# Performance work log

Measured on AMD Instinct MI355X. Metric: run time of the kernel, lower is better.

The kernel has to match this reference:

```python
import jax, jax.numpy as jnp
import numpy as np

B, L, HID, H, DH, M = 4, 4096, 1024, 16, 64, 128
EPS = 1e-3  # numerical_stabilizer


def setup_inputs() -> dict:
    key = jax.random.key(0)
    ks = jax.random.split(key, 7)
    lim = float(np.sqrt(6.0 / (HID + HID)))
    return {
        "query_input": jax.random.normal(ks[0], (B, L, HID), jnp.float32),
        "source_input": jax.random.normal(ks[1], (B, L, HID), jnp.float32),
        "Wq": jax.random.uniform(ks[2], (HID, H, DH), jnp.float32, -lim, lim),
        "Wk": jax.random.uniform(ks[3], (HID, H, DH), jnp.float32, -lim, lim),
        "Wv": jax.random.uniform(ks[4], (HID, H, DH), jnp.float32, -lim, lim),
        "Wo": jax.random.uniform(ks[5], (H, DH, HID), jnp.float32, -lim, lim),
        "proj": jax.random.normal(ks[6], (M, DH), jnp.float32),
        "training": 0,
    }


def _relu_kernel(x, proj):
    # relu_kernel_transformation: ratio * relu(x @ proj^T) + eps, [B,L,H,M]
    ratio = 1.0 / float(np.sqrt(proj.shape[0]))
    return jax.nn.relu(ratio * jnp.einsum("blhd,md->blhm", x, proj)) + EPS


def reference(query_input, source_input, Wq, Wk, Wv, Wo, proj, training):
    # QKV projections (DenseEinsum, no bias): [B,L,HID] -> [B,L,H,DH]
    q = jnp.einsum("bld,dhk->blhk", query_input, Wq)
    k = jnp.einsum("bld,dhk->blhk", source_input, Wk)
    v = jnp.einsum("bld,dhk->blhk", source_input, Wv)

    qp = _relu_kernel(q, proj)  # [B,L,H,M]
    kp = _relu_kernel(k, proj)  # [B,L,H,M]

    # noncausal FAVOR+: numerator via kv aggregation, linear in L
    kvs = jnp.einsum("blhm,blhd->bhmd", kp, v)          # [B,H,M,DH]
    num = jnp.einsum("blhm,bhmd->blhd", qp, kvs)        # [B,L,H,DH]
    ks_sum = jnp.sum(kp, axis=1)                         # [B,H,M]
    den = jnp.einsum("blhm,bhm->blh", qp, ks_sum)       # [B,L,H]
    att = num / den[..., None]                           # [B,L,H,DH]

    # output projection: [B,L,H,DH] -> [B,L,HID]
    return jnp.einsum("blhd,hdk->blk", att, Wo)
```

## Files before the change

### kernel.cpp

```cpp
#include <hip/hip_runtime.h>
#include <hip/hip_bf16.h>

#define B_   4
#define L_   4096
#define HID_ 1024
#define H_   16
#define DH_  64
#define M_   128
#define BL_  (B_*L_)
#define NROW (BL_*H_)

using short8 = __attribute__((ext_vector_type(8))) short;
using f32x4  = __attribute__((ext_vector_type(4))) float;

__device__ __forceinline__ float b2f(ushort s) {
    return __builtin_bit_cast(float, (unsigned int)s << 16);
}
__device__ __forceinline__ ushort f2b(float f) {
    unsigned int u = __builtin_bit_cast(unsigned int, f);
    u += 0x7fffu + ((u >> 16) & 1u);
    return (ushort)(u >> 16);
}

__device__ __forceinline__ void gld16(void* lds, const void* g) {
    __builtin_amdgcn_global_load_lds(
        (const __attribute__((address_space(1))) unsigned int*)g,
        (__attribute__((address_space(3))) unsigned int*)lds, 16, 0, 0);
}

__device__ __forceinline__ void xcd_swz_4x64(int& bx, int& by) {
    int orig = (int)blockIdx.x + ((int)blockIdx.y << 2);
    int nu = ((orig & 7) << 5) + (orig >> 3);
    bx = nu & 3; by = nu >> 2;
}

__device__ __forceinline__ void xcd_swz_8x128(int& bx, int& by) {
    int orig = (int)blockIdx.x + ((int)blockIdx.y << 3);
    int nu = ((orig & 7) << 7) + (orig >> 3);
    bx = nu & 7; by = nu >> 3;
}

__device__ __forceinline__ void gemm256_core(
    const ushort* __restrict__ A, const ushort* __restrict__ BT,
    int sA, int sB, ushort* LA, ushort* LB, f32x4 acc[8][4])
{
    const int t = threadIdx.x, w = t >> 6, lane = t & 63;
    const int wm = w >> 2, wn = w & 3, kg = lane >> 4, lr = lane & 15;
    const ushort* ga = A  + (size_t)lane * sA + w * 8;
    const ushort* gb = BT + (size_t)lane * sB + w * 8;
    ushort* la = LA + (size_t)(w * 256) * 8;
    ushort* lb = LB + (size_t)(w * 256) * 8;

    auto stageA = [&](int buf, int kt) {
        const ushort* g = ga + kt * 64;
        ushort* l = la + buf * 16384;
        #pragma unroll
        for (int j = 0; j < 4; ++j)
            gld16(l + (size_t)j * 512, g + (size_t)j * 64 * sA);
    };
    auto stageB = [&](int buf, int kt) {
        const ushort* g = gb + kt * 64;
        ushort* l = lb + buf * 16384;
        #pragma unroll
        for (int j = 0; j < 4; ++j)
            gld16(l + (size_t)j * 512, g + (size_t)j * 64 * sB);
    };
    auto compute = [&](int buf, int q) {
        const int kk = q >> 1, mh = q & 1;
        const ushort* lA_ = LA + buf * 16384;
        const ushort* lB_ = LB + buf * 16384;
        short8 av[4], bv[4];
        #pragma unroll
        for (int i = 0; i < 4; ++i)
            av[i] = *(const short8*)(lA_ +
                ((size_t)(kk*4 + kg)*256 + wm*128 + mh*64 + i*16 + lr) * 8);
        #pragma unroll
        for (int i = 0; i < 4; ++i)
            bv[i] = *(const short8*)(lB_ +
                ((size_t)(kk*4 + kg)*256 + wn*64 + i*16 + lr) * 8);
        __builtin_amdgcn_s_setprio(1);
        #pragma unroll
        for (int i = 0; i < 4; ++i)
            #pragma unroll
            for (int j = 0; j < 4; ++j)
                acc[mh*4 + i][j] = __builtin_amdgcn_mfma_f32_16x16x32_bf16(
                    av[i], bv[j], acc[mh*4 + i][j], 0, 0, 0);
        __builtin_amdgcn_s_setprio(0);
    };

    stageA(0, 0); stageB(0, 0);
    for (int kt = 0; kt < 16; ++kt) {
        const int buf = kt & 1;
        __syncthreads();
        compute(buf, 0);
        if (kt < 15) stageA(buf ^ 1, kt + 1);
        compute(buf, 1);
        if (kt < 15) stageB(buf ^ 1, kt + 1);
        compute(buf, 2);
        compute(buf, 3);
    }
    __syncthreads();
}

__device__ __forceinline__ void zero84(f32x4 acc[8][4]) {
    const f32x4 z4 = {0.f, 0.f, 0.f, 0.f};
    #pragma unroll
    for (int i = 0; i < 8; ++i)
        #pragma unroll
        for (int j = 0; j < 4; ++j) acc[i][j] = z4;
}

__global__ __launch_bounds__(512) void gemm_phi_mfma256(
    const ushort* __restrict__ A, const ushort* __restrict__ BT,
    const float* __restrict__ proj, ushort* __restrict__ OUT)
{
    __shared__ __align__(16) ushort lds[65536];
    int bx, by; xcd_swz_4x64(bx, by);
    const int bm = by * 256, bn = bx * 256, h0 = bx * 4;

    f32x4 acc[8][4];
    zero84(acc);
    gemm256_core(A + (size_t)bm * HID_, BT + (size_t)bn * HID_,
                 HID_, HID_, lds, lds + 32768, acc);

    const int t = threadIdx.x, w = t >> 6, lane = t & 63;
    const int wm = w >> 2, wn = w & 3, lr = lane & 15, rq = lane >> 4;

    short8 pbv[2][2];
    #pragma unroll
    for (int kk = 0; kk < 2; ++kk)
        #pragma unroll
        for (int n2 = 0; n2 < 2; ++n2) {
            const float* p = proj + (size_t)(wn*32 + n2*16 + lr) * DH_
                                  + (kk*4 + rq) * 8;
            float4 x = *(const float4*)p, y = *(const float4*)(p + 4);
            short8 v;
            v[0]=(short)f2b(x.x); v[1]=(short)f2b(x.y);
            v[2]=(short)f2b(x.z); v[3]=(short)f2b(x.w);
            v[4]=(short)f2b(y.x); v[5]=(short)f2b(y.y);
            v[6]=(short)f2b(y.z); v[7]=(short)f2b(y.w);
            pbv[kk][n2] = v;
        }

    #pragma unroll
    for (int mt = 0; mt < 8; ++mt)
        #pragma unroll
        for (int nt = 0; nt < 4; ++nt)
            #pragma unroll
            for (int p = 0; p < 4; ++p) {
                int row = wm*128 + mt*16 + rq*4 + p;
                int d   = nt*16 + lr;
                lds[(size_t)wn*16384 + ((size_t)(d>>3)*256 + row)*8 + (d&7)]
                    = f2b(acc[mt][nt][p]);
            }
    __syncthreads();

    const float ratio = 0.08838834764831845f;
    #pragma unroll
    for (int hs = 0; hs < 4; ++hs) {
        f32x4 a2[8][2];
        const f32x4 z4 = {0.f, 0.f, 0.f, 0.f};
        #pragma unroll
        for (int i = 0; i < 8; ++i) { a2[i][0] = z4; a2[i][1] = z4; }
        #pragma unroll
        for (int kk = 0; kk < 2; ++kk)
            #pragma unroll
            for (int mt = 0; mt < 8; ++mt) {
                short8 av = *(const short8*)(lds + (size_t)hs*16384 +
                    ((size_t)(kk*4 + rq)*256 + wm*128 + mt*16 + lr) * 8);
                #pragma unroll
                for (int n2 = 0; n2 < 2; ++n2)
                    a2[mt][n2] = __builtin_amdgcn_mfma_f32_16x16x32_bf16(
                        av, pbv[kk][n2], a2[mt][n2], 0, 0, 0);
            }
        #pragma unroll
        for (int mt = 0; mt < 8; ++mt)
            #pragma unroll
            for (int n2 = 0; n2 < 2; ++n2)
                #pragma unroll
                for (int p = 0; p < 4; ++p) {
                    size_t rowg = bm + wm*128 + mt*16 + rq*4 + p;
                    int m = wn*32 + n2*16 + lr;
                    float v = fmaxf(a2[mt][n2][p] * ratio, 0.f) + 1e-3f;
                    OUT[(rowg * H_ + (h0 + hs)) * M_ + m] = f2b(v);
                }
    }
}

__global__ __launch_bounds__(512) void gemm256_bf16(
    const ushort* __restrict__ A, const ushort* __restrict__ BT,
    ushort* __restrict__ C)
{
    __shared__ __align__(16) ushort lds[65536];
    int bx, by; xcd_swz_4x64(bx, by);
    const int bm = by * 256, bn = bx * 256;
    f32x4 acc[8][4];
    zero84(acc);
    gemm256_core(A + (size_t)bm * HID_, BT + (size_t)bn * HID_,
                 HID_, HID_, lds, lds + 32768, acc);
    const int t = threadIdx.x, w = t >> 6, lane = t & 63;
    const int wm = w >> 2, wn = w & 3, lr = lane & 15, rq = lane >> 4;
    #pragma unroll
    for (int mt = 0; mt < 8; ++mt)
        #pragma unroll
        for (int nt = 0; nt < 4; ++nt)
            #pragma unroll
            for (int p = 0; p < 4; ++p) {
                size_t row = bm + wm*128 + mt*16 + rq*4 + p;
                int col = bn + wn*64 + nt*16 + lr;
                C[row * HID_ + col] = f2b(acc[mt][nt][p]);
            }
}

__global__ __launch_bounds__(512) void gemm256_f32(
    const ushort* __restrict__ A, const ushort* __restrict__ BT,
    float* __restrict__ C)
{
    __shared__ __align__(16) ushort lds[65536];
    int bx, by; xcd_swz_4x64(bx, by);
    const int bm = by * 256, bn = bx * 256;
    f32x4 acc[8][4];
    zero84(acc);
    gemm256_core(A + (size_t)bm * HID_, BT + (size_t)bn * HID_,
                 HID_, HID_, lds, lds + 32768, acc);
    const int t = threadIdx.x, w = t >> 6, lane = t & 63;
    const int wm = w >> 2, wn = w & 3, lr = lane & 15, rq = lane >> 4;
    #pragma unroll
    for (int mt = 0; mt < 8; ++mt)
        #pragma unroll
        for (int nt = 0; nt < 4; ++nt)
            #pragma unroll
            for (int p = 0; p < 4; ++p) {
                size_t row = bm + wm*128 + mt*16 + rq*4 + p;
                int col = bn + wn*64 + nt*16 + lr;
                C[row * HID_ + col] = acc[mt][nt][p];
            }
}

__device__ __forceinline__ void mfma_gemm_g(
    const ushort* __restrict__ A, const ushort* __restrict__ BT,
    int sA, int sB, int K, ushort* As, ushort* Bs, f32x4 acc[4][4])
{
    const int t = threadIdx.x, w = t >> 6, lane = t & 63;
    const int wm = w >> 1, wn = w & 1, kg = lane >> 4, lr = lane & 15;
    const ushort* a0 = A  + (size_t)lane * sA + w * 8;
    const ushort* a1 = A  + (size_t)(64 + lane) * sA + w * 8;
    const ushort* b0 = BT + (size_t)lane * sB + w * 8;
    const ushort* b1 = BT + (size_t)(64 + lane) * sB + w * 8;
    ushort* lA0 = As + (size_t)(w * 128) * 8;
    ushort* lA1 = As + (size_t)(w * 128 + 64) * 8;
    ushort* lB0 = Bs + (size_t)(w * 128) * 8;
    ushort* lB1 = Bs + (size_t)(w * 128 + 64) * 8;

    gld16(lA0, a0); gld16(lA1, a1); gld16(lB0, b0); gld16(lB1, b1);
    __syncthreads();

    int cur = 0;
    for (int k0 = 0; k0 < K; k0 += 32) {
        const int nxt = cur ^ 1;
        if (k0 + 32 < K) {
            gld16(lA0 + nxt * 4096, a0 + k0 + 32);
            gld16(lA1 + nxt * 4096, a1 + k0 + 32);
            gld16(lB0 + nxt * 4096, b0 + k0 + 32);
            gld16(lB1 + nxt * 4096, b1 + k0 + 32);
        }
        const ushort* Ac = As + cur * 4096;
        const ushort* Bc = Bs + cur * 4096;
        short8 av[4], bv[4];
        #pragma unroll
        for (int i = 0; i < 4; ++i)
            av[i] = *(const short8*)(Ac + ((size_t)kg*128 + wm*64 + i*16 + lr) * 8);
        #pragma unroll
        for (int i = 0; i < 4; ++i)
            bv[i] = *(const short8*)(Bc + ((size_t)kg*128 + wn*64 + i*16 + lr) * 8);
        #pragma unroll
        for (int mt = 0; mt < 4; ++mt)
            #pragma unroll
            for (int nt = 0; nt < 4; ++nt)
                acc[mt][nt] = __builtin_amdgcn_mfma_f32_16x16x32_bf16(
                    av[mt], bv[nt], acc[mt][nt], 0, 0, 0);
        __syncthreads();
        cur = nxt;
    }
}

__global__ __launch_bounds__(256) void cvt_bf16(
    const float* __restrict__ X, ushort* __restrict__ Y, int n4)
{
    for (int i = blockIdx.x * 256 + threadIdx.x; i < n4; i += gridDim.x * 256) {
        float4 v = ((const float4*)X)[i];
        ushort4 o;
        o.x = f2b(v.x); o.y = f2b(v.y); o.z = f2b(v.z); o.w = f2b(v.w);
        ((ushort4*)Y)[i] = o;
    }
}

__global__ __launch_bounds__(256) void wtrans(
    const float* __restrict__ W, ushort* __restrict__ WT)
{
    __shared__ float tile[64][65];
    const int k0 = blockIdx.y * 64, n0 = blockIdx.x * 64;
    const int t = threadIdx.x;
    for (int i = t; i < 1024; i += 256) {
        int r = i >> 4, c4 = i & 15;
        float4 v = *(const float4*)(W + (size_t)(k0 + r) * HID_ + n0 + c4 * 4);
        tile[r][c4*4+0] = v.x; tile[r][c4*4+1] = v.y;
        tile[r][c4*4+2] = v.z; tile[r][c4*4+3] = v.w;
    }
    __syncthreads();
    for (int i = t; i < 1024; i += 256) {
        int n = i >> 4, c4 = i & 15;
        ushort4 o;
        o.x = f2b(tile[c4*4+0][n]); o.y = f2b(tile[c4*4+1][n]);
        o.z = f2b(tile[c4*4+2][n]); o.w = f2b(tile[c4*4+3][n]);
        *(ushort4*)(WT + (size_t)(n0 + n) * HID_ + k0 + c4 * 4) = o;
    }
}

__global__ __launch_bounds__(256) void kptrans_kernel(
    const ushort* __restrict__ KP, ushort* __restrict__ KPt,
    float* __restrict__ ksp)
{
    __shared__ __align__(16) ushort tile[128*128];
    const int bh = blockIdx.x, lc = blockIdx.y;
    const int b = bh >> 4, h = bh & 15;
    const int t = threadIdx.x;
    const size_t src = ((size_t)(b*L_ + lc*128) * H_ + h) * M_;

    #pragma unroll
    for (int it = 0; it < 8; ++it) {
        int i = it*256 + t;
        int l = i >> 4, mq = i & 15;
        int pb = mq ^ (l >> 3);
        *(uint4*)&tile[l*128 + pb*8] =
            *(const uint4*)&KP[src + (size_t)l*(H_*M_) + mq*8];
    }
    __syncthreads();

    if (t < 128) {
        float s = 0.f;
        for (int l = 0; l < 128; ++l) {
            int pb = (t >> 3) ^ (l >> 3);
            s += b2f(tile[l*128 + pb*8 + (t & 7)]);
        }
        ksp[((size_t)bh*32 + lc)*128 + t] = s;
    }

    #pragma unroll
    for (int it = 0; it < 8; ++it) {
        int i = it*256 + t;
        int m = i >> 4, lq = i & 15;
        short8 v;
        #pragma unroll
        for (int j = 0; j < 8; ++j) {
            int l = lq*8 + j;
            int pb = (m >> 3) ^ lq;
            v[j] = (short)tile[l*128 + pb*8 + (m & 7)];
        }
        *(short8*)&KPt[((size_t)bh*128 + m)*L_ + lc*128 + lq*8] = v;
    }
}

__global__ __launch_bounds__(256) void vtrans_kernel(
    const ushort* __restrict__ V, ushort* __restrict__ Vt)
{
    __shared__ __align__(16) ushort tile[128*64];
    const int bh = blockIdx.x, lc = blockIdx.y;
    const int b = bh >> 4, h = bh & 15;
    const int t = threadIdx.x;
    const size_t src = ((size_t)(b*L_ + lc*128) * H_ + h) * DH_;

    #pragma unroll
    for (int it = 0; it < 4; ++it) {
        int i = it*256 + t;
        int l = i >> 3, mq = i & 7;
        int pb = mq ^ ((l >> 3) & 7);
        *(uint4*)&tile[l*64 + pb*8] =
            *(const uint4*)&V[src + (size_t)l*(H_*DH_) + mq*8];
    }
    __syncthreads();

    #pragma unroll
    for (int it = 0; it < 4; ++it) {
        int i = it*256 + t;
        int d = i >> 4, lq = i & 15;
        short8 v;
        #pragma unroll
        for (int j = 0; j < 8; ++j) {
            int l = lq*8 + j;
            int pb = (d >> 3) ^ (lq & 7);
            v[j] = (short)tile[l*64 + pb*8 + (d & 7)];
        }
        *(short8*)&Vt[((size_t)bh*64 + d)*L_ + lc*128 + lq*8] = v;
    }
}

__global__ __launch_bounds__(256) void kvs_mfma(
    const ushort* __restrict__ Vt, const ushort* __restrict__ KPt,
    float* __restrict__ KVSP)
{
    __shared__ __align__(16) ushort As[4096], Bs[8192];
    const int bh = blockIdx.x, part = blockIdx.y;
    const ushort* A  = Vt  + (size_t)bh * 64  * L_ + part * 512;
    const ushort* BT = KPt + (size_t)bh * 128 * L_ + part * 512;
    const int t = threadIdx.x, w = t >> 6, lane = t & 63;
    const int wm = w >> 1, wn = w & 1, kg = lane >> 4, lr = lane & 15;
    const ushort* a0 = A  + (size_t)lane * L_ + w * 8;
    const ushort* b0 = BT + (size_t)lane * L_ + w * 8;
    const ushort* b1 = BT + (size_t)(64 + lane) * L_ + w * 8;
    ushort* lA0 = As + (size_t)(w * 64) * 8;
    ushort* lB0 = Bs + (size_t)(w * 128) * 8;
    ushort* lB1 = Bs + (size_t)(w * 128 + 64) * 8;

    f32x4 acc[2][4];
    const f32x4 z4 = {0.f, 0.f, 0.f, 0.f};
    #pragma unroll
    for (int mt = 0; mt < 2; ++mt)
        #pragma unroll
        for (int nt = 0; nt < 4; ++nt) acc[mt][nt] = z4;

    gld16(lA0, a0); gld16(lB0, b0); gld16(lB1, b1);
    __syncthreads();

    int cur = 0;
    for (int k0 = 0; k0 < 512; k0 += 32) {
        const int nxt = cur ^ 1;
        if (k0 + 32 < 512) {
            gld16(lA0 + nxt * 2048, a0 + k0 + 32);
            gld16(lB0 + nxt * 4096, b0 + k0 + 32);
            gld16(lB1 + nxt * 4096, b1 + k0 + 32);
        }
        const ushort* Ac = As + cur * 2048;
        const ushort* Bc = Bs + cur * 4096;
        short8 av[2], bv[4];
        #pragma unroll
        for (int i = 0; i < 2; ++i)
            av[i] = *(const short8*)(Ac + ((size_t)kg*64 + wm*32 + i*16 + lr) * 8);
        #pragma unroll
        for (int i = 0; i < 4; ++i)
            bv[i] = *(const short8*)(Bc + ((size_t)kg*128 + wn*64 + i*16 + lr) * 8);
        #pragma unroll
        for (int mt = 0; mt < 2; ++mt)
            #pragma unroll
            for (int nt = 0; nt < 4; ++nt)
                acc[mt][nt] = __builtin_amdgcn_mfma_f32_16x16x32_bf16(
                    av[mt], bv[nt], acc[mt][nt], 0, 0, 0);
        __syncthreads();
        cur = nxt;
    }

    const int rq = lane >> 4;
    #pragma unroll
    for (int mt = 0; mt < 2; ++mt)
        #pragma unroll
        for (int nt = 0; nt < 4; ++nt)
            #pragma unroll
            for (int p = 0; p < 4; ++p) {
                int row = wm*32 + mt*16 + rq*4 + p;
                int col = wn*64 + nt*16 + lr;
                KVSP[(((size_t)part*64 + bh)*64 + row)*128 + col]
                    = acc[mt][nt][p];
            }
}

__global__ __launch_bounds__(256) void kvs_reduce_kernel(
    const float* __restrict__ KVSP, const float* __restrict__ ksp,
    ushort* __restrict__ KVSt)
{
    const int bh = blockIdx.x;
    for (int i = threadIdx.x; i < 128*128; i += 256) {
        int d = i >> 7, m = i & 127;
        ushort v = 0;
        if (d < 64) {
            float s = 0.f;
            #pragma unroll
            for (int p = 0; p < 8; ++p)
                s += KVSP[(((size_t)p*64 + bh)*64 + d)*128 + m];
            v = f2b(s);
        } else if (d == 64) {
            float s = 0.f;
            #pragma unroll
            for (int c = 0; c < 32; ++c)
                s += ksp[((size_t)bh*32 + c)*128 + m];
            v = f2b(s);
        }
        KVSt[(size_t)bh * 16384 + i] = v;
    }
}

__global__ __launch_bounds__(256) void numden_mfma(
    const ushort* __restrict__ QP, const ushort* __restrict__ KVSt,
    ushort* __restrict__ ATT)
{
    __shared__ __align__(16) ushort As[8192], Bs[8192];
    __shared__ float sden[128];
    const int bh = blockIdx.x, b = bh >> 4, h = bh & 15;
    const int l0 = blockIdx.y * 128;
    const ushort* Abase = QP + ((size_t)(b * L_ + l0) * H_ + h) * M_;
    const ushort* Bbase = KVSt + (size_t)bh * 16384;

    f32x4 acc[4][4];
    const f32x4 z4 = {0.f, 0.f, 0.f, 0.f};
    #pragma unroll
    for (int mt = 0; mt < 4; ++mt)
        #pragma unroll
        for (int nt = 0; nt < 4; ++nt) acc[mt][nt] = z4;

    mfma_gemm_g(Abase, Bbase, H_*M_, 128, 128, As, Bs, acc);

    const int t = threadIdx.x, w = t >> 6, lane = t & 63;
    const int wm = w >> 1, wn = w & 1, lr = lane & 15, rq = lane >> 4;

    if (wn == 1 && lr == 0) {
        #pragma unroll
        for (int mt = 0; mt < 4; ++mt)
            #pragma unroll
            for (int p = 0; p < 4; ++p)
                sden[wm*64 + mt*16 + rq*4 + p] = acc[mt][0][p];
    }
    __syncthreads();

    if (wn == 0) {
        #pragma unroll
        for (int mt = 0; mt < 4; ++mt) {
            #pragma unroll
            for (int p = 0; p < 4; ++p) {
                int row = wm*64 + mt*16 + rq*4 + p;
                float den = fmaxf(sden[row], 1e-10f);
                float rden = 1.0f / den;
                size_t gbase = (size_t)(b * L_ + l0 + row) * HID_ + h * DH_;
                #pragma unroll
                for (int nt = 0; nt < 4; ++nt)
                    ATT[gbase + nt*16 + lr] = f2b(acc[mt][nt][p] * rden);
            }
        }
    }
}

extern "C" void kernel_launch(void* const* d_in, const int* in_sizes, int n_in,
                              void* d_out, int out_size, void* d_ws, size_t ws_size,
                              hipStream_t stream)
{
    const float* Xq = (const float*)d_in[0];
    const float* Xs = (const float*)d_in[1];
    const float* Wq = (const float*)d_in[2];
    const float* Wk = (const float*)d_in[3];
    const float* Wv = (const float*)d_in[4];
    const float* Wo = (const float*)d_in[5];
    const float* Pj = (const float*)d_in[6];
    float* out = (float*)d_out;

    char* ws = (char*)d_ws;
    ushort* WqT = (ushort*)(ws + 0);
    ushort* WkT = (ushort*)(ws + 2097152);
    ushort* WvT = (ushort*)(ws + 4194304);
    ushort* WoT = (ushort*)(ws + 6291456);
    ushort* Xqb = (ushort*)(ws + 8388608);
    ushort* Xsb = (ushort*)(ws + 41943040);
    ushort* QPb = (ushort*)(ws + 75497472);
    ushort* KPb = (ushort*)(ws + 142606336);
    ushort* Vb  = (ushort*)(ws + 209715200);
    ushort* KPt = (ushort*)(ws + 8388608);
    ushort* Vt  = (ushort*)(ws + 142606336);
    float*  KVSP = (float*)(ws + 176160768);
    ushort* KVSt = (ushort*)(ws + 192937984);
    float*  ksp  = (float*)(ws + 0);
    ushort* ATT  = Vb;

    dim3 tb(256);
    dim3 tb512(512);

    cvt_bf16<<<4096, tb, 0, stream>>>(Xq, Xqb, BL_*HID_/4);
    cvt_bf16<<<4096, tb, 0, stream>>>(Xs, Xsb, BL_*HID_/4);
    wtrans<<<dim3(16,16), tb, 0, stream>>>(Wq, WqT);
    wtrans<<<dim3(16,16), tb, 0, stream>>>(Wk, WkT);
    wtrans<<<dim3(16,16), tb, 0, stream>>>(Wv, WvT);
    wtrans<<<dim3(16,16), tb, 0, stream>>>(Wo, WoT);

    gemm_phi_mfma256<<<dim3(4, 64), tb512, 0, stream>>>(Xqb, WqT, Pj, QPb);
    gemm_phi_mfma256<<<dim3(4, 64), tb512, 0, stream>>>(Xsb, WkT, Pj, KPb);
    gemm256_bf16<<<dim3(4, 64), tb512, 0, stream>>>(Xsb, WvT, Vb);

    kptrans_kernel<<<dim3(64, 32), tb, 0, stream>>>(KPb, KPt, ksp);
    vtrans_kernel<<<dim3(64, 32), tb, 0, stream>>>(Vb, Vt);

    kvs_mfma<<<dim3(64, 8), tb, 0, stream>>>(Vt, KPt, KVSP);
    kvs_reduce_kernel<<<64, tb, 0, stream>>>(KVSP, ksp, KVSt);

    numden_mfma<<<dim3(B_*H_, L_/128), tb, 0, stream>>>(QPb, KVSt, ATT);

    gemm256_f32<<<dim3(4, 64), tb512, 0, stream>>>(ATT, WoT, out);
    (void)in_sizes; (void)n_in; (void)out_size; (void)ws_size;
}
```

Measured before the change: 511.7 us.

## Restructure 256x256 GEMM core into quadrant-pipelined schedule with fine-grained vmcnt waits

Rewrites the shared 256x256 bf16 MFMA GEMM core so that each K-step is split into four 128x128 quadrants. The prefetch of the next stage's A/B halves is interleaved between quadrant computes, with explicit s_waitcnt vmcnt and raw s_barrier instead of full __syncthreads. The warp tile mapping changes to a 2x2 quadrant layout, and all epilogues (phi kernel LDS transpose, bf16 and f32 stores) are remapped to match. The aim is to overlap global-to-LDS loads with MFMA work and reduce barrier stalls. In exchange, the hand-tuned wait counts are fragile and the remapped epilogue index math could introduce layout bugs.

```diff
diff --git a/kernel.cpp b/kernel.cpp
--- a/kernel.cpp
+++ b/kernel.cpp
@@ -28,86 +28,115 @@
         (__attribute__((address_space(3))) unsigned int*)lds, 16, 0, 0);
 }
 
+#define VMCNT4 asm volatile("s_waitcnt vmcnt(4)" ::: "memory")
+#define VMCNT2 asm volatile("s_waitcnt vmcnt(2)" ::: "memory")
+#define VMCNT0 asm volatile("s_waitcnt vmcnt(0)" ::: "memory")
+#define SBAR do { __builtin_amdgcn_sched_barrier(0); \
+                  __builtin_amdgcn_s_barrier(); \
+                  __builtin_amdgcn_sched_barrier(0); } while (0)
+
 __device__ __forceinline__ void xcd_swz_4x64(int& bx, int& by) {
     int orig = (int)blockIdx.x + ((int)blockIdx.y << 2);
     int nu = ((orig & 7) << 5) + (orig >> 3);
     bx = nu & 3; by = nu >> 2;
 }
 
-__device__ __forceinline__ void xcd_swz_8x128(int& bx, int& by) {
-    int orig = (int)blockIdx.x + ((int)blockIdx.y << 3);
-    int nu = ((orig & 7) << 7) + (orig >> 3);
-    bx = nu & 7; by = nu >> 3;
-}
-
 __device__ __forceinline__ void gemm256_core(
     const ushort* __restrict__ A, const ushort* __restrict__ BT,
-    int sA, int sB, ushort* LA, ushort* LB, f32x4 acc[8][4])
+    int sA, int sB, ushort* lds, f32x4 acc[2][2][4][2])
 {
     const int t = threadIdx.x, w = t >> 6, lane = t & 63;
-    const int wm = w >> 2, wn = w & 3, kg = lane >> 4, lr = lane & 15;
-    const ushort* ga = A  + (size_t)lane * sA + w * 8;
-    const ushort* gb = BT + (size_t)lane * sB + w * 8;
-    ushort* la = LA + (size_t)(w * 256) * 8;
-    ushort* lb = LB + (size_t)(w * 256) * 8;
-
-    auto stageA = [&](int buf, int kt) {
-        const ushort* g = ga + kt * 64;
-        ushort* l = la + buf * 16384;
-        #pragma unroll
-        for (int j = 0; j < 4; ++j)
-            gld16(l + (size_t)j * 512, g + (size_t)j * 64 * sA);
+    const int wr = (w >> 2) & 1, wc = w & 3, kg = lane >> 4, lr = lane & 15;
+    ushort* LA = lds;
+    ushort* LB = lds + 32768;
+
+    auto stageA = [&](int b, int hf, int kt) {
+        ushort* l = LA + ((size_t)((b*2 + hf)*8 + w)) * 1024;
+        const ushort* g = A + (size_t)(hf*128 + lane) * sA + kt*64 + w*8;
+        gld16(l,       g);
+        gld16(l + 512, g + (size_t)64 * sA);
     };
-    auto stageB = [&](int buf, int kt) {
-        const ushort* g = gb + kt * 64;
-        ushort* l = lb + buf * 16384;
-        #pragma unroll
-        for (int j = 0; j < 4; ++j)
-            gld16(l + (size_t)j * 512, g + (size_t)j * 64 * sB);
+    auto stageB = [&](int b, int hf, int kt) {
+        ushort* l = LB + ((size_t)((b*2 + hf)*8 + w)) * 1024;
+        const ushort* g = BT + (size_t)(hf*128 + lane) * sB + kt*64 + w*8;
+        gld16(l,       g);
+        gld16(l + 512, g + (size_t)64 * sB);
     };
-    auto compute = [&](int buf, int q) {
-        const int kk = q >> 1, mh = q & 1;
-        const ushort* lA_ = LA + buf * 16384;
-        const ushort* lB_ = LB + buf * 16384;
-        short8 av[4], bv[4];
-        #pragma unroll
-        for (int i = 0; i < 4; ++i)
-            av[i] = *(const short8*)(lA_ +
-                ((size_t)(kk*4 + kg)*256 + wm*128 + mh*64 + i*16 + lr) * 8);
-        #pragma unroll
-        for (int i = 0; i < 4; ++i)
-            bv[i] = *(const short8*)(lB_ +
-                ((size_t)(kk*4 + kg)*256 + wn*64 + i*16 + lr) * 8);
+
+    short8 av[2][4], bv[2][2];
+    auto loadA = [&](int b, int r) {
+        #pragma unroll
+        for (int kk = 0; kk < 2; ++kk)
+            #pragma unroll
+            for (int i = 0; i < 4; ++i)
+                av[kk][i] = *(const short8*)(LA
+                    + ((size_t)((b*2 + r)*8 + kk*4 + kg)) * 1024
+                    + (size_t)(wr*64 + i*16 + lr) * 8);
+    };
+    auto loadB = [&](int b, int c) {
+        #pragma unroll
+        for (int kk = 0; kk < 2; ++kk)
+            #pragma unroll
+            for (int j = 0; j < 2; ++j)
+                bv[kk][j] = *(const short8*)(LB
+                    + ((size_t)((b*2 + c)*8 + kk*4 + kg)) * 1024
+                    + (size_t)(wc*32 + j*16 + lr) * 8);
+    };
+    auto mfma16 = [&](int r, int c) {
         __builtin_amdgcn_s_setprio(1);
         #pragma unroll
-        for (int i = 0; i < 4; ++i)
-            #pragma unroll
-            for (int j = 0; j < 4; ++j)
-                acc[mh*4 + i][j] = __builtin_amdgcn_mfma_f32_16x16x32_bf16(
-                    av[i], bv[j], acc[mh*4 + i][j], 0, 0, 0);
+        for (int kk = 0; kk < 2; ++kk)
+            #pragma unroll
+            for (int i = 0; i < 4; ++i)
+                #pragma unroll
+                for (int j = 0; j < 2; ++j)
+                    acc[r][c][i][j] = __builtin_amdgcn_mfma_f32_16x16x32_bf16(
+                        av[kk][i], bv[kk][j], acc[r][c][i][j], 0, 0, 0);
         __builtin_amdgcn_s_setprio(0);
     };
 
-    stageA(0, 0); stageB(0, 0);
-    for (int kt = 0; kt < 16; ++kt) {
-        const int buf = kt & 1;
-        __syncthreads();
-        compute(buf, 0);
-        if (kt < 15) stageA(buf ^ 1, kt + 1);
-        compute(buf, 1);
-        if (kt < 15) stageB(buf ^ 1, kt + 1);
-        compute(buf, 2);
-        compute(buf, 3);
-    }
-    __syncthreads();
-}
-
-__device__ __forceinline__ void zero84(f32x4 acc[8][4]) {
+    stageA(0, 0, 0); stageB(0, 0, 0); stageB(0, 1, 0); stageA(0, 1, 0);
+
+    for (int kt = 0; kt < 15; ++kt) {
+        const int b = kt & 1, nb = b ^ 1;
+        VMCNT4; SBAR;
+        loadA(b, 0); loadB(b, 0);
+        stageA(nb, 0, kt + 1);
+        mfma16(0, 0);
+        VMCNT4; SBAR;
+        loadB(b, 1);
+        stageB(nb, 0, kt + 1);
+        mfma16(0, 1);
+        VMCNT4; SBAR;
+        loadA(b, 1);
+        stageB(nb, 1, kt + 1);
+        mfma16(1, 1);
+        loadB(b, 0);
+        stageA(nb, 1, kt + 1);
+        mfma16(1, 0);
+    }
+    {
+        VMCNT4; SBAR;
+        loadA(1, 0); loadB(1, 0); mfma16(0, 0);
+        VMCNT2; SBAR;
+        loadB(1, 1); mfma16(0, 1);
+        VMCNT0; SBAR;
+        loadA(1, 1); mfma16(1, 1);
+        loadB(1, 0); mfma16(1, 0);
+    }
+    __syncthreads();
+}
+
+__device__ __forceinline__ void zero224(f32x4 acc[2][2][4][2]) {
     const f32x4 z4 = {0.f, 0.f, 0.f, 0.f};
     #pragma unroll
-    for (int i = 0; i < 8; ++i)
-        #pragma unroll
-        for (int j = 0; j < 4; ++j) acc[i][j] = z4;
+    for (int r = 0; r < 2; ++r)
+        #pragma unroll
+        for (int c = 0; c < 2; ++c)
+            #pragma unroll
+            for (int i = 0; i < 4; ++i)
+                #pragma unroll
+                for (int j = 0; j < 2; ++j) acc[r][c][i][j] = z4;
 }
 
 __global__ __launch_bounds__(512) void gemm_phi_mfma256(
@@ -118,20 +147,20 @@
     int bx, by; xcd_swz_4x64(bx, by);
     const int bm = by * 256, bn = bx * 256, h0 = bx * 4;
 
-    f32x4 acc[8][4];
-    zero84(acc);
+    f32x4 acc[2][2][4][2];
+    zero224(acc);
     gemm256_core(A + (size_t)bm * HID_, BT + (size_t)bn * HID_,
-                 HID_, HID_, lds, lds + 32768, acc);
+                 HID_, HID_, lds, acc);
 
     const int t = threadIdx.x, w = t >> 6, lane = t & 63;
-    const int wm = w >> 2, wn = w & 3, lr = lane & 15, rq = lane >> 4;
+    const int wr = (w >> 2) & 1, wc = w & 3, lr = lane & 15, rq = lane >> 4;
 
     short8 pbv[2][2];
     #pragma unroll
     for (int kk = 0; kk < 2; ++kk)
         #pragma unroll
         for (int n2 = 0; n2 < 2; ++n2) {
-            const float* p = proj + (size_t)(wn*32 + n2*16 + lr) * DH_
+            const float* p = proj + (size_t)(wc*32 + n2*16 + lr) * DH_
                                   + (kk*4 + rq) * 8;
             float4 x = *(const float4*)p, y = *(const float4*)(p + 4);
             short8 v;
@@ -143,19 +172,25 @@
         }
 
     #pragma unroll
-    for (int mt = 0; mt < 8; ++mt)
-        #pragma unroll
-        for (int nt = 0; nt < 4; ++nt)
-            #pragma unroll
-            for (int p = 0; p < 4; ++p) {
-                int row = wm*128 + mt*16 + rq*4 + p;
-                int d   = nt*16 + lr;
-                lds[(size_t)wn*16384 + ((size_t)(d>>3)*256 + row)*8 + (d&7)]
-                    = f2b(acc[mt][nt][p]);
-            }
+    for (int r = 0; r < 2; ++r)
+        #pragma unroll
+        for (int c = 0; c < 2; ++c)
+            #pragma unroll
+            for (int i = 0; i < 4; ++i)
+                #pragma unroll
+                for (int j = 0; j < 2; ++j)
+                    #pragma unroll
+                    for (int p = 0; p < 4; ++p) {
+                        int row = r*128 + wr*64 + i*16 + rq*4 + p;
+                        int hs  = c*2 + (wc >> 1);
+                        int d   = (wc & 1)*32 + j*16 + lr;
+                        lds[(size_t)hs*16384 + ((size_t)(d>>3)*256 + row)*8 + (d&7)]
+                            = f2b(acc[r][c][i][j][p]);
+                    }
     __syncthreads();
 
     const float ratio = 0.08838834764831845f;
+    const int wm = w >> 2;
     #pragma unroll
     for (int hs = 0; hs < 4; ++hs) {
         f32x4 a2[8][2];
@@ -180,7 +215,7 @@
                 #pragma unroll
                 for (int p = 0; p < 4; ++p) {
                     size_t rowg = bm + wm*128 + mt*16 + rq*4 + p;
-                    int m = wn*32 + n2*16 + lr;
+                    int m = wc*32 + n2*16 + lr;
                     float v = fmaxf(a2[mt][n2][p] * ratio, 0.f) + 1e-3f;
                     OUT[(rowg * H_ + (h0 + hs)) * M_ + m] = f2b(v);
                 }
@@ -194,22 +229,26 @@
     __shared__ __align__(16) ushort lds[65536];
     int bx, by; xcd_swz_4x64(bx, by);
     const int bm = by * 256, bn = bx * 256;
-    f32x4 acc[8][4];
-    zero84(acc);
+    f32x4 acc[2][2][4][2];
+    zero224(acc);
     gemm256_core(A + (size_t)bm * HID_, BT + (size_t)bn * HID_,
-                 HID_, HID_, lds, lds + 32768, acc);
+                 HID_, HID_, lds, acc);
     const int t = threadIdx.x, w = t >> 6, lane = t & 63;
-    const int wm = w >> 2, wn = w & 3, lr = lane & 15, rq = lane >> 4;
-    #pragma unroll
-    for (int mt = 0; mt < 8; ++mt)
-        #pragma unroll
-        for (int nt = 0; nt < 4; ++nt)
-            #pragma unroll
-            for (int p = 0; p < 4; ++p) {
-                size_t row = bm + wm*128 + mt*16 + rq*4 + p;
-                int col = bn + wn*64 + nt*16 + lr;
-                C[row * HID_ + col] = f2b(acc[mt][nt][p]);
-            }
+    const int wr = (w >> 2) & 1, wc = w & 3, lr = lane & 15, rq = lane >> 4;
+    #pragma unroll
+    for (int r = 0; r < 2; ++r)
+        #pragma unroll
+        for (int c = 0; c < 2; ++c)
+            #pragma unroll
+            for (int i = 0; i < 4; ++i)
+                #pragma unroll
+                for (int j = 0; j < 2; ++j)
+                    #pragma unroll
+                    for (int p = 0; p < 4; ++p) {
+                        size_t row = bm + r*128 + wr*64 + i*16 + rq*4 + p;
+                        int col = bn + c*128 + wc*32 + j*16 + lr;
+                        C[row * HID_ + col] = f2b(acc[r][c][i][j][p]);
+                    }
 }
 
 __global__ __launch_bounds__(512) void gemm256_f32(
@@ -219,22 +258,26 @@
     __shared__ __align__(16) ushort lds[65536];
     int bx, by; xcd_swz_4x64(bx, by);
     const int bm = by * 256, bn = bx * 256;
-    f32x4 acc[8][4];
-    zero84(acc);
+    f32x4 acc[2][2][4][2];
+    zero224(acc);
     gemm256_core(A + (size_t)bm * HID_, BT + (size_t)bn * HID_,
-                 HID_, HID_, lds, lds + 32768, acc);
+                 HID_, HID_, lds, acc);
     const int t = threadIdx.x, w = t >> 6, lane = t & 63;
-    const int wm = w >> 2, wn = w & 3, lr = lane & 15, rq = lane >> 4;
-    #pragma unroll
-    for (int mt = 0; mt < 8; ++mt)
-        #pragma unroll
-        for (int nt = 0; nt < 4; ++nt)
-            #pragma unroll
-            for (int p = 0; p < 4; ++p) {
-                size_t row = bm + wm*128 + mt*16 + rq*4 + p;
-                int col = bn + wn*64 + nt*16 + lr;
-                C[row * HID_ + col] = acc[mt][nt][p];
-            }
+    const int wr = (w >> 2) & 1, wc = w & 3, lr = lane & 15, rq = lane >> 4;
+    #pragma unroll
+    for (int r = 0; r < 2; ++r)
+        #pragma unroll
+        for (int c = 0; c < 2; ++c)
+            #pragma unroll
+            for (int i = 0; i < 4; ++i)
+                #pragma unroll
+                for (int j = 0; j < 2; ++j)
+                    #pragma unroll
+                    for (int p = 0; p < 4; ++p) {
+                        size_t row = bm + r*128 + wr*64 + i*16 + rq*4 + p;
+                        int col = bn + c*128 + wc*32 + j*16 + lr;
+                        C[row * HID_ + col] = acc[r][c][i][j][p];
+                    }
 }
 
 __device__ __forceinline__ void mfma_gemm_g(
```

Result: faster. 483.4 us (-5.5%).
